# Kernel tuning notes

Hardware: AMD Instinct MI355X
Metric: run time of the kernel (lower is better)

The kernel has to match this reference:

```python
import jax, jax.numpy as jnp
import numpy as np

B, S, E, H, VS, VT = 128, 256, 512, 512, 32000, 32000


def _lstm_layer(x, mask, Wih, Whh, bih, bhh):
    # x: (S,B,E_in), mask: (S,B) bool. PyTorch gate order i,f,g,o.
    h0 = jnp.zeros((x.shape[1], Whh.shape[1]), x.dtype)
    c0 = h0
    def step(carry, inp):
        h, c = carry
        xt, mt = inp
        g = xt @ Wih.T + h @ Whh.T + bih + bhh
        i, f, gg, o = jnp.split(g, 4, axis=-1)
        i = jax.nn.sigmoid(i); f = jax.nn.sigmoid(f)
        gg = jnp.tanh(gg); o = jax.nn.sigmoid(o)
        c_new = f * c + i * gg
        h_new = o * jnp.tanh(c_new)
        m = mt[:, None]
        h2 = jnp.where(m, h_new, h)
        c2 = jnp.where(m, c_new, c)
        return (h2, c2), jnp.where(m, h_new, 0.0)  # pad_packed zero-pads
    (hT, cT), ys = jax.lax.scan(step, (h0, c0), (x, mask))
    return ys, cT


def setup_inputs() -> dict:
    key = jax.random.key(0)
    ks = jax.random.split(key, 32)
    def w(k, shape, fan_in):
        bound = 1.0 / np.sqrt(fan_in)
        return jax.random.uniform(k, shape, jnp.float32, -bound, bound)
    src_tokens = jax.random.randint(ks[0], (B, S), 0, VS)
    src_lens = jnp.sort(jax.random.randint(ks[1], (B,), S // 2, S + 1))[::-1]
    src_lens = src_lens.at[0].set(S)  # pack_padded expects descending, max = S
    trg_tokens = jax.random.randint(ks[2], (B,), 0, VT)
    inp = {
        'src_tokens': src_tokens, 'src_lens': src_lens, 'trg_tokens': trg_tokens,
        'src_emb': jax.random.normal(ks[3], (VS, E), jnp.float32),
        'trg_emb': jax.random.normal(ks[4], (VT, E), jnp.float32),
        'enc_Wih0': w(ks[5], (4 * H, E), H), 'enc_Whh0': w(ks[6], (4 * H, H), H),
        'enc_bih0': w(ks[7], (4 * H,), H), 'enc_bhh0': w(ks[8], (4 * H,), H),
        'enc_Wih1': w(ks[9], (4 * H, H), H), 'enc_Whh1': w(ks[10], (4 * H, H), H),
        'enc_bih1': w(ks[11], (4 * H,), H), 'enc_bhh1': w(ks[12], (4 * H,), H),
        'dec_Wih': w(ks[13], (4 * H, E + H), H), 'dec_Whh': w(ks[14], (4 * H, H), H),
        'dec_bih': w(ks[15], (4 * H,), H), 'dec_bhh': w(ks[16], (4 * H,), H),
        'W_init': w(ks[17], (H, 2 * H), 2 * H), 'b_init': w(ks[18], (H,), 2 * H),
        'W_hid': w(ks[19], (H, 2 * H), 2 * H), 'b_hid': w(ks[20], (H,), 2 * H),
        'W_out': w(ks[21], (VT, H), H), 'b_out': w(ks[22], (VT,), H),
    }
    return inp


def reference(src_tokens, src_lens, trg_tokens, src_emb, trg_emb,
              enc_Wih0, enc_Whh0, enc_bih0, enc_bhh0,
              enc_Wih1, enc_Whh1, enc_bih1, enc_bhh1,
              dec_Wih, dec_Whh, dec_bih, dec_bhh,
              W_init, b_init, W_hid, b_hid, W_out, b_out):
    # ---- encode ----
    x = src_emb[src_tokens]                       # (B,S,E)
    x = jnp.transpose(x, (1, 0, 2))               # (S,B,E)
    mask = jnp.arange(S)[:, None] < src_lens[None, :]  # (S,B)
    y0, c0f = _lstm_layer(x, mask, enc_Wih0, enc_Whh0, enc_bih0, enc_bhh0)
    y1, c1f = _lstm_layer(y0, mask, enc_Wih1, enc_Whh1, enc_bih1, enc_bhh1)
    src_states = jnp.transpose(y1, (1, 0, 2))     # (B,S,H)
    # final cell states (num_layers,B,H) -> (B, num_layers*H)
    final_cells = jnp.concatenate([c0f, c1f], axis=-1)  # (B,2H)
    c_dec = final_cells @ W_init.T + b_init       # (B,H)
    h_dec = jnp.tanh(c_dec)
    # ---- one decoder step ----
    emb_t = trg_emb[trg_tokens]                   # (B,E)
    vec = jnp.concatenate([emb_t, jnp.zeros((B, H), emb_t.dtype)], axis=-1)
    g = vec @ dec_Wih.T + h_dec @ dec_Whh.T + dec_bih + dec_bhh
    i, f, gg, o = jnp.split(g, 4, axis=-1)
    c = jax.nn.sigmoid(f) * c_dec + jax.nn.sigmoid(i) * jnp.tanh(gg)
    h = jax.nn.sigmoid(o) * jnp.tanh(c)           # (B,H)
    # ---- masked dot attention ----
    scores = jnp.einsum('bsh,bh->bs', src_states, h)
    smask = jnp.arange(S)[None, :] < src_lens[:, None]
    scores = jnp.where(smask, scores, -jnp.inf)
    attw = jax.nn.softmax(scores, axis=-1)
    context = jnp.einsum('bs,bsh->bh', attw, src_states)
    attn_vec = jnp.concatenate([h, context], axis=-1) @ W_hid.T + b_hid
    logits = attn_vec @ W_out.T + b_out
    prd_token = jnp.argmax(logits, axis=-1)       # softmax is monotone
    return context, h, prd_token
```

## Files before the change

kernel.cpp:

```cpp
#include <hip/hip_runtime.h>
#include <stdint.h>


typedef _Float16 f16;
typedef f16 f16x8 __attribute__((ext_vector_type(8)));
typedef float f32x4 __attribute__((ext_vector_type(4)));

#define LOSCALE 2048.0f
#define LOINV   (1.0f/2048.0f)

#define B_  128
#define S_  256
#define H_  512

__device__ __forceinline__ uint16_t hbits(f16 h){ union{ f16 f; uint16_t u; } c; c.f=h; return c.u; }

__device__ __forceinline__ uint32_t split_ph2(float x){
  f16 h = (f16)x;
  float r = (x - (float)h) * LOSCALE;
  return (uint32_t)hbits(h) | ((uint32_t)hbits((f16)r) << 16);
}
__device__ __forceinline__ float ph2val(uint32_t p){
  union{ uint16_t u; f16 f; } a, b; a.u = (uint16_t)p; b.u = (uint16_t)(p>>16);
  return (float)a.f + (float)b.f * LOINV;
}

__device__ __forceinline__ void pack_hi_lo(const uint4& a, const uint4& b, uint4& hi, uint4& lo){
  hi = make_uint4((a.x & 0xffffu) | (a.y << 16),
                  (a.z & 0xffffu) | (a.w << 16),
                  (b.x & 0xffffu) | (b.y << 16),
                  (b.z & 0xffffu) | (b.w << 16));
  lo = make_uint4((a.x >> 16) | (a.y & 0xffff0000u),
                  (a.z >> 16) | (a.w & 0xffff0000u),
                  (b.x >> 16) | (b.y & 0xffff0000u),
                  (b.z >> 16) | (b.w & 0xffff0000u));
}

__device__ __forceinline__ void split_pack8(const float* x, uint4& hi, uint4& lo){
  uint16_t h[8], l[8];
#pragma unroll
  for (int e = 0; e < 8; ++e) {
    f16 hh = (f16)x[e];
    float r = (x[e] - (float)hh) * LOSCALE;
    h[e] = hbits(hh); l[e] = hbits((f16)r);
  }
  hi = make_uint4((uint32_t)h[0]|((uint32_t)h[1]<<16), (uint32_t)h[2]|((uint32_t)h[3]<<16),
                  (uint32_t)h[4]|((uint32_t)h[5]<<16), (uint32_t)h[6]|((uint32_t)h[7]<<16));
  lo = make_uint4((uint32_t)l[0]|((uint32_t)l[1]<<16), (uint32_t)l[2]|((uint32_t)l[3]<<16),
// ... 5 lines not shown
      __builtin_bit_cast(f16x8, a), __builtin_bit_cast(f16x8, b), c, 0, 0, 0);
}

__device__ __forceinline__ float sigm(float x){ return 1.0f/(1.0f + expf(-x)); }
__device__ __forceinline__ float fsigm(float x){ return 1.0f/(1.0f + __expf(-x)); }
__device__ __forceinline__ float ftanh(float x){
  float ax = fabsf(x);
  float e = __expf(-2.0f*ax);
  float r = (1.0f - e)/(1.0f + e);
  return copysignf(r, x);
}

__device__ __forceinline__ uint32_t plane_word(uint32_t p, uint32_t pp, int odd){
  return odd ? ((pp >> 16) | (p & 0xffff0000u))
             : ((p & 0xffffu) | (pp << 16));
}

__device__ __forceinline__ size_t fl_idx(int row, int k){
  return (size_t)(k >> 5) * 4096 + (size_t)(row >> 4) * 512 + (size_t)(k & 1) * 256
       + (size_t)((k >> 3) & 3) * 64 + (size_t)(row & 15) * 4 + (size_t)((k & 7) >> 1);
}

__device__ __forceinline__ void gload_lds16(const uint32_t* gbase, uint32_t* lbase, int lane){
#if __has_builtin(__builtin_amdgcn_global_load_lds)
  __builtin_amdgcn_global_load_lds(
      (const __attribute__((address_space(1))) uint32_t*)(gbase + lane*4),
      (__attribute__((address_space(3))) uint32_t*)lbase, 16, 0, 0);
#else
  *(uint4*)(lbase + lane*4) = *(const uint4*)(gbase + lane*4);
#endif
}

__global__ __launch_bounds__(256) void k_embed_src_fl(const int* __restrict__ tok,
    const float* __restrict__ emb, uint32_t* __restrict__ out)
{
  const size_t total = (size_t)S_ * B_ * H_;
  for (size_t i = (size_t)blockIdx.x*256 + threadIdx.x; i < total; i += (size_t)gridDim.x*256) {
    int s = (int)(i >> 16), b = (int)((i >> 9) & 127), k = (int)(i & 511);
    int t = tok[b*S_ + s];
    uint32_t p = split_ph2(emb[(size_t)t*H_ + k]);
    uint32_t pp = __shfl_xor(p, 1);
    out[(size_t)s*65536 + fl_idx(b, k)] = plane_word(p, pp, k & 1);
  }
}

__global__ __launch_bounds__(256) void k_embed_trg(const int* __restrict__ tok,
    const float* __restrict__ emb, uint32_t* __restrict__ out)
{
  int i = blockIdx.x*256 + threadIdx.x;
  int e = i & (H_-1), b = i >> 9;
  int t = tok[b];
  out[i] = split_ph2(emb[(size_t)t*H_ + e]);
}

__global__ __launch_bounds__(256) void k_packW(const float* __restrict__ W,
    uint32_t* __restrict__ out)
{
  int i = blockIdx.x*256 + threadIdx.x;
  int n = i >> 9, k = i & 511;
  uint32_t p = split_ph2(W[i]);
  uint32_t pp = __shfl_xor(p, 1);
  out[(size_t)(n >> 7)*65536 + fl_idx(n & 127, k)] = plane_word(p, pp, k & 1);
}

__global__ __launch_bounds__(256) void k_packAfl(const float* __restrict__ a,
    uint32_t* __restrict__ out)
{
  int i = blockIdx.x*256 + threadIdx.x;
  int b = i >> 9, k = i & 511;
  uint32_t p = split_ph2(a[i]);
  uint32_t pp = __shfl_xor(p, 1);
  out[fl_idx(b, k)] = plane_word(p, pp, k & 1);
}

__global__ __launch_bounds__(256,2) void k_gemm_fl(
    const uint32_t* __restrict__ Afl,
    const uint32_t* __restrict__ Wfl,
    const float* __restrict__ b0, const float* __restrict__ b1,
    float* __restrict__ C, int N, int addC)
{
  __shared__ uint8_t sm[65536];
  const int tid = threadIdx.x, lane = tid & 63, wv = tid >> 6;
  const int wm = wv >> 1, wn = wv & 1;
  const int bn0 = blockIdx.x * 128, bm0 = blockIdx.y * 128;
  const uint32_t* Ab = Afl + (size_t)blockIdx.y * 65536;
  const uint32_t* Wb = Wfl + (size_t)blockIdx.x * 65536;

  f32x4 acc0[4][4], acc1[4][4];
#pragma unroll
  for (int i = 0; i < 4; ++i)
#pragma unroll
    for (int j = 0; j < 4; ++j) { acc0[i][j] = (f32x4){0,0,0,0}; acc1[i][j] = (f32x4){0,0,0,0}; }

  for (int it = 0; it < 8; ++it) {
    __syncthreads();
    {
      const uint32_t* gsrc = (wv < 2 ? Ab : Wb) + (size_t)it*8192 + (size_t)(wv & 1)*4096;
      uint32_t* lb = (uint32_t*)(sm + (size_t)wv*16384);
#pragma unroll
      for (int e = 0; e < 16; ++e)
        gload_lds16(gsrc + e*256, lb + e*256, lane);
    }
    asm volatile("s_waitcnt vmcnt(0)" ::: "memory");
    __syncthreads();

#pragma unroll
    for (int kt = 0; kt < 2; ++kt) {
      uint4 ah[4], al[4];
#pragma unroll
      for (int i = 0; i < 4; ++i) {
        const uint8_t* p = sm + (size_t)(kt*8 + wm*4 + i)*2048 + lane*16;
        ah[i] = *(const uint4*)p; al[i] = *(const uint4*)(p + 1024);
      }
#pragma unroll
      for (int j = 0; j < 4; ++j) {
        const uint8_t* p = sm + 32768 + (size_t)(kt*8 + wn*4 + j)*2048 + lane*16;
        uint4 bh = *(const uint4*)p;
        uint4 bl = *(const uint4*)(p + 1024);
#pragma unroll
        for (int i = 0; i < 4; ++i) {
          acc0[i][j] = mfma16(ah[i], bh, acc0[i][j]);
          acc1[i][j] = mfma16(al[i], bh, acc1[i][j]);
          acc1[i][j] = mfma16(ah[i], bl, acc1[i][j]);
        }
      }
    }
  }

#pragma unroll
  for (int i = 0; i < 4; ++i) {
    int row0 = bm0 + (wm*4+i)*16 + ((lane>>4)<<2);
#pragma unroll
    for (int j = 0; j < 4; ++j) {
      int col = bn0 + (wn*4+j)*16 + (lane & 15);
      float bias = 0.f;
      if (b0) bias += b0[col];
      if (b1) bias += b1[col];
      f32x4 v = acc0[i][j] + acc1[i][j] * LOINV;
#pragma unroll
      for (int r = 0; r < 4; ++r) {
        size_t idx = (size_t)(row0 + r) * N + col;
        float out = v[r] + bias;
        if (addC) out += C[idx];
        C[idx] = out;
      }
    }
  }
}

__global__ __launch_bounds__(256,2) void k_gemm(
    const uint32_t* __restrict__ A, int lda,
    const float* __restrict__ W, int ldw,
    const float* __restrict__ b0, const float* __restrict__ b1,
    float* __restrict__ C, int N, int K, int addC)
{
  __shared__ uint8_t sm[65536];
  const int tid = threadIdx.x;
  const int lane = tid & 63, wv = tid >> 6;
  const int wm = wv >> 1, wn = wv & 1;
  const int bn0 = blockIdx.x * 128, bm0 = blockIdx.y * 128;

  const int srow = tid >> 1;
  const int skh  = (tid & 1) * 32;
  const int smt  = srow >> 4, sr = srow & 15, skt = tid & 1;

  f32x4 acc0[4][4], acc1[4][4];
#pragma unroll
  for (int i = 0; i < 4; ++i)
#pragma unroll
    for (int j = 0; j < 4; ++j) { acc0[i][j] = (f32x4){0,0,0,0}; acc1[i][j] = (f32x4){0,0,0,0}; }

  for (int k0 = 0; k0 < K; k0 += 64) {
    __syncthreads();
    {
      const uint32_t* ap = A + (size_t)(bm0 + srow) * lda + (k0 + skh);
      uint4 q[8];
#pragma unroll
// ... 34 lines not shown
        uint4 bh = *(const uint4*)p;
        uint4 bl = *(const uint4*)(p + 1024);
#pragma unroll
        for (int i = 0; i < 4; ++i) {
          acc0[i][j] = mfma16(ah[i], bh, acc0[i][j]);
          acc1[i][j] = mfma16(al[i], bh, acc1[i][j]);
          acc1[i][j] = mfma16(ah[i], bl, acc1[i][j]);
        }
      }
    }
  }

#pragma unroll
  for (int i = 0; i < 4; ++i) {
    int row0 = bm0 + (wm*4+i)*16 + ((lane>>4)<<2);
#pragma unroll
    for (int j = 0; j < 4; ++j) {
      int col = bn0 + (wn*4+j)*16 + (lane & 15);
      float bias = 0.f;
      if (b0) bias += b0[col];
      if (b1) bias += b1[col];
      f32x4 v = acc0[i][j] + acc1[i][j] * LOINV;
#pragma unroll
      for (int r = 0; r < 4; ++r) {
        size_t idx = (size_t)(row0 + r) * N + col;
        float out = v[r] + bias;
        if (addC) out += C[idx];
        C[idx] = out;
      }
    }
  }
}

__global__ __launch_bounds__(256,1) void k_lstm2(
    const float* __restrict__ Whh0, const float* __restrict__ Whh1,
    const float* __restrict__ bih1, const float* __restrict__ bhh1,
    const float* __restrict__ xg,
    const int*  __restrict__ lens,
    uint32_t* __restrict__ mb0,
    uint32_t* __restrict__ mb1,
    float* __restrict__ cb0, float* __restrict__ cb1,
    uint32_t* __restrict__ y1buf,
    uint32_t* __restrict__ flg0, uint32_t* __restrict__ flg1,
    const uint32_t* __restrict__ Wp1,
    int s0, int nt)
{
  __shared__ uint8_t sm[163840];
  uint8_t* wih = sm;
  uint8_t* tile = sm + 131072;
  uint64_t* tile64 = (uint64_t*)tile;
  float* g0ex = (float*)tile;
  float* g1ex = (float*)(tile + 4096);

  const int tid = threadIdx.x, lane = tid & 63, wv = tid >> 6;
  const int bg = blockIdx.x & 7, hs = blockIdx.x >> 3;
  const int row = lane & 15, qh = lane >> 4;

  {
    const uint32_t* wpb = Wp1 + (size_t)(wv*4 + (hs >> 3))*65536 + (size_t)(hs & 7)*512;
    uint32_t* lb = (uint32_t*)(wih + (size_t)wv*32768);
#pragma unroll
    for (int kt = 0; kt < 16; ++kt) {
      gload_lds16(wpb + kt*4096,       lb + kt*512,       lane);
      gload_lds16(wpb + kt*4096 + 256, lb + kt*512 + 256, lane);
    }
  }

  uint4 w0h[16], w0l[16], w1h[16], w1l[16];
  {
    const float* r0 = Whh0 + (size_t)(wv*512 + hs*16 + row)*512 + qh*8;
    const float* r1 = Whh1 + (size_t)(wv*512 + hs*16 + row)*512 + qh*8;
#pragma unroll
    for (int kt = 0; kt < 16; ++kt) {
      float xs[8];
      float4 v0 = *(const float4*)(r0 + kt*32), v1 = *(const float4*)(r0 + kt*32 + 4);
      xs[0]=v0.x; xs[1]=v0.y; xs[2]=v0.z; xs[3]=v0.w;
      xs[4]=v1.x; xs[5]=v1.y; xs[6]=v1.z; xs[7]=v1.w;
      split_pack8(xs, w0h[kt], w0l[kt]);
      v0 = *(const float4*)(r1 + kt*32); v1 = *(const float4*)(r1 + kt*32 + 4);
      xs[0]=v0.x; xs[1]=v0.y; xs[2]=v0.z; xs[3]=v0.w;
      xs[4]=v1.x; xs[5]=v1.y; xs[6]=v1.z; xs[7]=v1.w;
      split_pack8(xs, w1h[kt], w1l[kt]);
    }
  }

  const int b_l = tid >> 4, uu = tid & 15;
  const int bglob = bg*16 + b_l;
  const size_t bgoff = (size_t)bg*8192;
  const int oct_p = hs*2 + (uu >> 3);
  const size_t widx = (size_t)b_l*512 + (size_t)(uu & 1)*256
                    + ((size_t)(oct_p ^ b_l) << 2) + (size_t)((uu & 7) >> 1);
  const int len_b = lens[bglob];
  const int lenA  = lens[bg*16 + row];
  float c0_reg = cb0[(size_t)bglob*512 + hs*16 + uu];
  float c1_reg = cb1[(size_t)bglob*512 + hs*16 + uu];
  float h0_reg, h1_reg;
  {
    size_t ib = (size_t)(s0 & 1)*65536 + bgoff + (size_t)b_l*512
              + ((size_t)(oct_p ^ b_l) << 2) + (size_t)((uu & 7) >> 1);
    uint32_t hiw = mb0[ib], low = mb0[ib + 256];
    int sh = (uu & 1) * 16;
    union{ uint16_t u; f16 f; } ch, cl;
    ch.u = (uint16_t)(hiw >> sh); cl.u = (uint16_t)(low >> sh);
    h0_reg = (float)ch.f + (float)cl.f * LOINV;
    int s1i = (s0 >= 1) ? (s0 - 1) : 0;
    size_t ib1 = (size_t)(s1i & 1)*65536 + bgoff + (size_t)b_l*512
               + ((size_t)(oct_p ^ b_l) << 2) + (size_t)((uu & 7) >> 1);
    hiw = mb1[ib1]; low = mb1[ib1 + 256];
    ch.u = (uint16_t)(hiw >> sh); cl.u = (uint16_t)(low >> sh);
    h1_reg = (float)ch.f + (float)cl.f * LOINV;
  }
  float b1g[4];
#pragma unroll
  for (int g = 0; g < 4; ++g)
    b1g[g] = bih1[g*512 + hs*16 + uu] + bhh1[g*512 + hs*16 + uu];
  const size_t yfl = (size_t)(hs >> 1)*4096 + (size_t)bg*512 + (size_t)(uu & 1)*256
                   + (size_t)((((hs & 1) << 1) | (uu >> 3)))*64 + (size_t)b_l*4
                   + (size_t)((uu & 7) >> 1);

  asm volatile("s_waitcnt vmcnt(0)" ::: "memory");
  __syncthreads();

  for (int it = 0; it < nt; ++it) {
    const int t = s0 + it;
    const bool aL0 = (t < 256);
    const bool aL1 = (t > 0);

    float xv0 = 0.f, xv1 = 0.f, xv2 = 0.f, xv3 = 0.f;
    if (aL0) {
      const float* xgp = xg + ((size_t)it*128 + bglob)*2048 + hs*16 + uu;
      xv0 = xgp[0]; xv1 = xgp[512]; xv2 = xgp[1024]; xv3 = xgp[1536];
    }

    if (it > 0) {
      if (wv == 0) {
        const uint32_t* fp = flg0 + bg*32 + (lane & 31);
        while (1) {
          uint32_t f = __hip_atomic_load(fp, __ATOMIC_RELAXED, __HIP_MEMORY_SCOPE_SYSTEM);
          if (__all((int)(f >= (uint32_t)t))) break;
          __builtin_amdgcn_s_sleep(1);
        }
      } else if (wv == 1) {
        const uint32_t* fp = flg1 + bg*32 + (lane & 31);
        while (1) {
          uint32_t f = __hip_atomic_load(fp, __ATOMIC_RELAXED, __HIP_MEMORY_SCOPE_SYSTEM);
          if (__all((int)(f >= (uint32_t)(t - 1)))) break;
          __builtin_amdgcn_s_sleep(1);
        }
      }
    }
    __builtin_amdgcn_s_barrier();
    __builtin_amdgcn_sched_barrier(0);

    const uint64_t* sp0 = (const uint64_t*)(mb0 + (size_t)(t & 1)*65536 + bgoff);
    const uint64_t* sp1 = (const uint64_t*)(mb1 + (size_t)((t - 1) & 1)*65536 + bgoff);
    uint64_t v0[16], v1[16];
#pragma unroll
    for (int e = 0; e < 16; ++e)
      v0[e] = __hip_atomic_load(sp0 + tid + e*256, __ATOMIC_RELAXED, __HIP_MEMORY_SCOPE_SYSTEM);
    if (aL1) {
#pragma unroll
      for (int e = 0; e < 16; ++e)
        v1[e] = __hip_atomic_load(sp1 + tid + e*256, __ATOMIC_RELAXED, __HIP_MEMORY_SCOPE_SYSTEM);
    }
#pragma unroll
    for (int e = 0; e < 16; ++e)
      tile64[tid + e*256] = v0[e];
    asm volatile("s_waitcnt lgkmcnt(0)" ::: "memory");
    __builtin_amdgcn_s_barrier();
    __builtin_amdgcn_sched_barrier(0);

    f32x4 A0 = (f32x4){0,0,0,0}, A1 = (f32x4){0,0,0,0}, A2 = (f32x4){0,0,0,0};
    f32x4 B0 = (f32x4){0,0,0,0}, B1 = (f32x4){0,0,0,0}, B2 = (f32x4){0,0,0,0};
    {
      const uint8_t* hrp = tile + (size_t)row*2048;
      const uint8_t* wbase = wih + (size_t)wv*32768;
      const bool cY = aL1 && ((t - 1) < lenA);
      const uint4 z4 = make_uint4(0,0,0,0);
#pragma unroll
      for (int kt = 0; kt < 16; ++kt) {
        int oct = kt*4 + qh;
        const uint8_t* pA = hrp + (((oct ^ row)) << 4);
        uint4 ah = *(const uint4*)pA, al = *(const uint4*)(pA + 1024);
        A0 = mfma16(ah, w0h[kt], A0);
        A1 = mfma16(al, w0h[kt], A1);
        A2 = mfma16(ah, w0l[kt], A2);
        uint4 yh = cY ? ah : z4, yl = cY ? al : z4;
        const uint8_t* pB = wbase + (size_t)kt*2048 + lane*16;
        uint4 bh = *(const uint4*)pB, bl = *(const uint4*)(pB + 1024);
        B0 = mfma16(yh, bh, B0);
        B1 = mfma16(yl, bh, B1);
        B2 = mfma16(yh, bl, B2);
      }
    }
    __builtin_amdgcn_sched_barrier(0);
    __builtin_amdgcn_s_barrier();
    __builtin_amdgcn_sched_barrier(0);

    if (aL1) {
#pragma unroll
      for (int e = 0; e < 16; ++e)
        tile64[tid + e*256] = v1[e];
    }
    asm volatile("s_waitcnt lgkmcnt(0)" ::: "memory");
    __builtin_amdgcn_s_barrier();
    __builtin_amdgcn_sched_barrier(0);

    if (aL1) {
      const uint8_t* hrp = tile + (size_t)row*2048;
#pragma unroll
      for (int kt = 0; kt < 16; ++kt) {
        int oct = kt*4 + qh;
        const uint8_t* pA = hrp + (((oct ^ row)) << 4);
        uint4 ah = *(const uint4*)pA, al = *(const uint4*)(pA + 1024);
        B0 = mfma16(ah, w1h[kt], B0);
        B1 = mfma16(al, w1h[kt], B1);
        B2 = mfma16(ah, w1l[kt], B2);
      }
    }
    __builtin_amdgcn_sched_barrier(0);
    __builtin_amdgcn_s_barrier();
    __builtin_amdgcn_sched_barrier(0);

    {
      int col = lane & 15, rb = (lane >> 4) << 2;
      if (aL0) {
#pragma unroll
        for (int r = 0; r < 4; ++r)
          g0ex[(size_t)(wv*16 + rb + r)*16 + col] = A0[r] + (A1[r] + A2[r])*LOINV;
      }
      if (aL1) {
#pragma unroll
        for (int r = 0; r < 4; ++r)
          g1ex[(size_t)(wv*16 + rb + r)*16 + col] = B0[r] + (B1[r] + B2[r])*LOINV;
      }
    }
    asm volatile("s_waitcnt lgkmcnt(0)" ::: "memory");
    __builtin_amdgcn_s_barrier();
    __builtin_amdgcn_sched_barrier(0);

    uint32_t p1w = 0; bool m1 = false;
    if (aL0) {
      float gi = g0ex[(size_t)(0*16 + b_l)*16 + uu] + xv0;
      float gf = g0ex[(size_t)(1*16 + b_l)*16 + uu] + xv1;
      float gg = g0ex[(size_t)(2*16 + b_l)*16 + uu] + xv2;
      float go = g0ex[(size_t)(3*16 + b_l)*16 + uu] + xv3;
      float cn = fsigm(gf)*c0_reg + fsigm(gi)*ftanh(gg);
      float hn = fsigm(go)*ftanh(cn);
      bool m = (t < len_b);
      c0_reg = m ? cn : c0_reg;
      h0_reg = m ? hn : h0_reg;
      uint32_t p = split_ph2(h0_reg);
      uint32_t pp = __shfl_xor(p, 1);
      __hip_atomic_store(mb0 + (size_t)((t + 1) & 1)*65536 + bgoff + widx,
                         plane_word(p, pp, uu & 1), __ATOMIC_RELAXED, __HIP_MEMORY_SCOPE_SYSTEM);
    }
    if (aL1) {
      float gi = g1ex[(size_t)(0*16 + b_l)*16 + uu] + b1g[0];
      float gf = g1ex[(size_t)(1*16 + b_l)*16 + uu] + b1g[1];
      float gg = g1ex[(size_t)(2*16 + b_l)*16 + uu] + b1g[2];
      float go = g1ex[(size_t)(3*16 + b_l)*16 + uu] + b1g[3];
      float cn = fsigm(gf)*c1_reg + fsigm(gi)*ftanh(gg);
      float hn = fsigm(go)*ftanh(cn);
      m1 = ((t - 1) < len_b);
      c1_reg = m1 ? cn : c1_reg;
      h1_reg = m1 ? hn : h1_reg;
      uint32_t p = split_ph2(h1_reg);
      uint32_t pp = __shfl_xor(p, 1);
      p1w = plane_word(p, pp, uu & 1);
      __hip_atomic_store(mb1 + (size_t)(t & 1)*65536 + bgoff + widx,
                         p1w, __ATOMIC_RELAXED, __HIP_MEMORY_SCOPE_SYSTEM);
    }
    asm volatile("s_waitcnt vmcnt(0)" ::: "memory");
    __builtin_amdgcn_s_barrier();
    __builtin_amdgcn_sched_barrier(0);
    if (tid == 0) {
      if (aL0) __hip_atomic_store(flg0 + bg*32 + hs, (uint32_t)(t + 1),
                                  __ATOMIC_RELAXED, __HIP_MEMORY_SCOPE_SYSTEM);
      if (aL1) __hip_atomic_store(flg1 + bg*32 + hs, (uint32_t)t,
                                  __ATOMIC_RELAXED, __HIP_MEMORY_SCOPE_SYSTEM);
    }
    if (aL1) y1buf[(size_t)(t - 1)*65536 + yfl] = m1 ? p1w : 0u;
  }
  cb0[(size_t)bglob*512 + hs*16 + uu] = c0_reg;
  cb1[(size_t)bglob*512 + hs*16 + uu] = c1_reg;
}

__global__ __launch_bounds__(256) void k_pack2(const float* __restrict__ a,
    const float* __restrict__ b, uint32_t* __restrict__ out)
{
  int i = blockIdx.x*256 + threadIdx.x;
  int bb = i >> 10, k = i & 1023;
  float x = (k < 512) ? a[(size_t)bb*512 + k] : b[(size_t)bb*512 + k - 512];
  out[i] = split_ph2(x);
}

__global__ __launch_bounds__(256) void k_tanh_split(const float* __restrict__ c,
    uint32_t* __restrict__ hp)
{ int i = blockIdx.x*256 + threadIdx.x; hp[i] = split_ph2(tanhf(c[i])); }

__global__ __launch_bounds__(256) void k_dec_cell(const float* __restrict__ g,
    const float* __restrict__ cdec, float* __restrict__ hout, float* __restrict__ dh)
{
  int i = blockIdx.x*256 + threadIdx.x;
  int b = i >> 9, u = i & 511;
  const float* gb = g + (size_t)b*2048;
  float c = sigm(gb[512 + u])*cdec[i] + sigm(gb[u])*tanhf(gb[1024 + u]);
  float h = sigm(gb[1536 + u])*tanhf(c);
  hout[i] = h; dh[i] = h;
}

__global__ __launch_bounds__(256) void k_attn(const uint32_t* __restrict__ y1,
    const float* __restrict__ h, const int* __restrict__ lens,
    float* __restrict__ ctx, float* __restrict__ dctx)
{
  __shared__ float hsh[512];
  __shared__ float sc[256];
  __shared__ float red[8];
  const int b = blockIdx.x, tid = threadIdx.x, lane = tid & 63, wv = tid >> 6;
  hsh[tid]       = h[(size_t)b*512 + tid];
  hsh[tid + 256] = h[(size_t)b*512 + tid + 256];
  const int len = lens[b];
  __syncthreads();

  const size_t lanebase = (size_t)(lane >> 2)*4096 + (size_t)(b >> 4)*512
                        + (size_t)(lane & 3)*64 + (size_t)(b & 15)*4;
  for (int it = 0; it < 64; ++it) {
    int s = wv*64 + it;
    const uint32_t* yb = y1 + (size_t)s*65536 + lanebase;
    uint4 hw = *(const uint4*)yb;
    uint4 lw = *(const uint4*)(yb + 256);
    int k0 = lane*8;
    uint32_t hws[4] = {hw.x,hw.y,hw.z,hw.w}, lws[4] = {lw.x,lw.y,lw.z,lw.w};
    float d = 0.f;
#pragma unroll
    for (int w = 0; w < 4; ++w) {
      union{uint16_t u; f16 f;} h0,h1,l0,l1;
      h0.u=(uint16_t)hws[w]; h1.u=(uint16_t)(hws[w]>>16);
      l0.u=(uint16_t)lws[w]; l1.u=(uint16_t)(lws[w]>>16);
      d += ((float)h0.f + (float)l0.f*LOINV) * hsh[k0 + 2*w]
         + ((float)h1.f + (float)l1.f*LOINV) * hsh[k0 + 2*w + 1];
    }
    for (int off = 32; off; off >>= 1) d += __shfl_xor(d, off);
    if (lane == 0) sc[s] = d;
  }
  __syncthreads();

  float v = (tid < len) ? sc[tid] : -INFINITY;
  float mx = v;
  for (int off = 32; off; off >>= 1) mx = fmaxf(mx, __shfl_xor(mx, off));
  if (lane == 0) red[wv] = mx;
  __syncthreads();
  mx = fmaxf(fmaxf(red[0], red[1]), fmaxf(red[2], red[3]));
  float e = (tid < len) ? expf(v - mx) : 0.f;
  float ssum = e;
  for (int off = 32; off; off >>= 1) ssum += __shfl_xor(ssum, off);
  if (lane == 0) red[4 + wv] = ssum;
  __syncthreads();
  float tot = red[4] + red[5] + red[6] + red[7];
  __syncthreads();
  sc[tid] = e / tot;
  __syncthreads();

  const int u0 = tid, u1 = tid + 256;
  const size_t bu0 = (size_t)(u0 >> 5)*4096 + (size_t)(b >> 4)*512
                   + (size_t)((u0 >> 3) & 3)*64 + (size_t)(b & 15)*4 + (size_t)((u0 & 7) >> 1);
  const size_t bu1 = (size_t)(u1 >> 5)*4096 + (size_t)(b >> 4)*512
                   + (size_t)((u1 >> 3) & 3)*64 + (size_t)(b & 15)*4 + (size_t)((u1 & 7) >> 1);
  const int sh = (tid & 1) * 16;
  float acc0 = 0.f, acc1 = 0.f;
  for (int s = 0; s < 256; ++s) {
    float w = sc[s];
    const uint32_t* yb = y1 + (size_t)s*65536;
    uint32_t hi0 = yb[bu0], lo0 = yb[bu0 + 256];
    uint32_t hi1 = yb[bu1], lo1 = yb[bu1 + 256];
    union{uint16_t u; f16 f;} a,b2,c2,d2;
    a.u =(uint16_t)(hi0 >> sh); b2.u=(uint16_t)(lo0 >> sh);
    c2.u=(uint16_t)(hi1 >> sh); d2.u=(uint16_t)(lo1 >> sh);
    acc0 += w*((float)a.f  + (float)b2.f*LOINV);
    acc1 += w*((float)c2.f + (float)d2.f*LOINV);
  }
  ctx [(size_t)b*512 + tid]       = acc0;  ctx [(size_t)b*512 + tid + 256] = acc1;
  dctx[(size_t)b*512 + tid]       = acc0;  dctx[(size_t)b*512 + tid + 256] = acc1;
}

__global__ __launch_bounds__(256) void k_argmax(const float* __restrict__ logits,
    float* __restrict__ out)
{
  __shared__ float bv[256];
  __shared__ int   bi[256];
  const int b = blockIdx.x, tid = threadIdx.x;
  const float* L = logits + (size_t)b*32000;
  float best = -INFINITY; int idx = 0;
  for (int i = tid; i < 32000; i += 256) {
    float v = L[i];
    if (v > best) { best = v; idx = i; }
  }
  bv[tid] = best; bi[tid] = idx;
  __syncthreads();
  for (int sft = 128; sft; sft >>= 1) {
    if (tid < sft) {
      if (bv[tid+sft] > bv[tid] || (bv[tid+sft] == bv[tid] && bi[tid+sft] < bi[tid])) {
        bv[tid] = bv[tid+sft]; bi[tid] = bi[tid+sft];
      }
    }
    __syncthreads();
  }
  if (tid == 0) out[b] = (float)bi[0];
}

extern "C" void kernel_launch(void* const* d_in, const int* in_sizes, int n_in,
                              void* d_out, int out_size, void* d_ws, size_t ws_size,
                              hipStream_t stream)
{
  (void)in_sizes; (void)n_in; (void)out_size; (void)ws_size;
  const int*   src_tokens = (const int*)  d_in[0];
  const int*   src_lens   = (const int*)  d_in[1];
  const int*   trg_tokens = (const int*)  d_in[2];
  const float* src_emb    = (const float*)d_in[3];
  const float* trg_emb    = (const float*)d_in[4];
  const float* Wih0 = (const float*)d_in[5];
  const float* Whh0 = (const float*)d_in[6];
  const float* bih0 = (const float*)d_in[7];
  const float* bhh0 = (const float*)d_in[8];
  const float* Wih1 = (const float*)d_in[9];
  const float* Whh1 = (const float*)d_in[10];
  const float* bih1 = (const float*)d_in[11];
  const float* bhh1 = (const float*)d_in[12];
  const float* dWih = (const float*)d_in[13];
  const float* dWhh = (const float*)d_in[14];
  const float* dbih = (const float*)d_in[15];
  const float* dbhh = (const float*)d_in[16];
  const float* Winit= (const float*)d_in[17];
  const float* binit= (const float*)d_in[18];
  const float* Whid = (const float*)d_in[19];
  const float* bhid = (const float*)d_in[20];
  const float* Wout = (const float*)d_in[21];
  const float* bout = (const float*)d_in[22];

  uint8_t* ws = (uint8_t*)d_ws;
  constexpr size_t MBs = 1ull << 20;
  constexpr size_t OFF_AP    = 0;
  constexpr size_t OFF_Y1    = 64*MBs;
  constexpr size_t OFF_XG    = 128*MBs;
  constexpr size_t OFF_MB    = 192*MBs;
  constexpr size_t OFF_CB0   = OFF_MB    + 1*MBs;
  constexpr size_t OFF_CB1   = OFF_CB0   + 256*1024;
  constexpr size_t OFF_FLG   = OFF_CB1   + 256*1024;
  constexpr size_t OFF_PK    = OFF_FLG   + 4096;
  constexpr size_t OFF_CDEC  = OFF_PK    + 512*1024;
  constexpr size_t OFF_HDECP = OFF_CDEC  + 256*1024;
  constexpr size_t OFF_EMBP  = OFF_HDECP + 256*1024;
  constexpr size_t OFF_G     = OFF_EMBP  + 256*1024;
  constexpr size_t OFF_HDEC2 = OFF_G     + 1*MBs;
  constexpr size_t OFF_CTX   = OFF_HDEC2 + 256*1024;
  constexpr size_t OFF_AVEC  = OFF_CTX   + 256*1024;
  constexpr size_t OFF_AVECP = OFF_AVEC  + 256*1024;
  constexpr size_t OFF_LOG   = OFF_AVECP + 256*1024;

  uint32_t* Ap    = (uint32_t*)(ws + OFF_AP);
  uint32_t* Y1    = (uint32_t*)(ws + OFF_Y1);
  float*    Xg    = (float*)   (ws + OFF_XG);
  uint32_t* WoutF = (uint32_t*)(ws + OFF_XG);
  uint32_t* mb0   = (uint32_t*)(ws + OFF_MB);
  uint32_t* mb1   = (uint32_t*)(ws + OFF_MB + 512*1024);
  float*    cb0   = (float*)   (ws + OFF_CB0);
  float*    cb1   = (float*)   (ws + OFF_CB1);
  uint32_t* flg0  = (uint32_t*)(ws + OFF_FLG);
  uint32_t* flg1  = (uint32_t*)(ws + OFF_FLG + 2048);
  uint32_t* pk    = (uint32_t*)(ws + OFF_PK);
  float*    cdec  = (float*)   (ws + OFF_CDEC);
  uint32_t* hdecp = (uint32_t*)(ws + OFF_HDECP);
  uint32_t* embp  = (uint32_t*)(ws + OFF_EMBP);
  float*    g     = (float*)   (ws + OFF_G);
  float*    hdec2 = (float*)   (ws + OFF_HDEC2);
  float*    ctx   = (float*)   (ws + OFF_CTX);
  float*    avec  = (float*)   (ws + OFF_AVEC);
  uint32_t* avecp = (uint32_t*)(ws + OFF_AVECP);
  float*    logit = (float*)   (ws + OFF_LOG);
  uint32_t* Wp0   = (uint32_t*)(ws + OFF_LOG);
  uint32_t* Wp1   = (uint32_t*)(ws + OFF_LOG + 4*MBs);
  float*    dout  = (float*)   d_out;

  k_packW<<<4096, 256, 0, stream>>>(Wih0, Wp0);
  k_packW<<<4096, 256, 0, stream>>>(Wih1, Wp1);

  hipMemsetAsync(mb0,  0, 1024*1024, stream);
  hipMemsetAsync(flg0, 0, 4096, stream);
  hipMemsetAsync(cb0,  0, 65536*4, stream);
  hipMemsetAsync(cb1,  0, 65536*4, stream);
  k_embed_src_fl<<<2048, 256, 0, stream>>>(src_tokens, src_emb, Ap);
  for (int c = 0; c < 4; ++c) {
    int s0 = c * 64;
    k_gemm_fl<<<dim3(16, 64), 256, 0, stream>>>(Ap + (size_t)s0*65536,
        Wp0, bih0, bhh0, Xg, 2048, 0);
    k_lstm2<<<256, 256, 0, stream>>>(Whh0, Whh1, bih1, bhh1, Xg, src_lens,
        mb0, mb1, cb0, cb1, Y1, flg0, flg1, Wp1, s0, (c == 3) ? 65 : 64);
  }

  k_packW<<<64000, 256, 0, stream>>>(Wout, WoutF);

  k_pack2<<<512, 256, 0, stream>>>(cb0, cb1, pk);
  k_gemm<<<dim3(4, 1), 256, 0, stream>>>(pk, 1024, Winit, 1024, binit, nullptr,
      cdec, 512, 1024, 0);
  k_tanh_split<<<256, 256, 0, stream>>>(cdec, hdecp);

  k_embed_trg<<<256, 256, 0, stream>>>(trg_tokens, trg_emb, embp);
  k_gemm<<<dim3(16, 1), 256, 0, stream>>>(embp, 512, dWih, 1024, dbih, dbhh,
      g, 2048, 512, 0);
  k_gemm<<<dim3(16, 1), 256, 0, stream>>>(hdecp, 512, dWhh, 512, nullptr, nullptr,
      g, 2048, 512, 1);
  k_dec_cell<<<256, 256, 0, stream>>>(g, cdec, hdec2, dout + 65536);

  k_attn<<<128, 256, 0, stream>>>(Y1, hdec2, src_lens, ctx, dout);

  k_pack2<<<512, 256, 0, stream>>>(hdec2, ctx, pk);
  k_gemm<<<dim3(4, 1), 256, 0, stream>>>(pk, 1024, Whid, 1024, bhid, nullptr,
      avec, 512, 1024, 0);
  k_packAfl<<<256, 256, 0, stream>>>(avec, avecp);
  k_gemm_fl<<<dim3(250, 1), 256, 0, stream>>>(avecp, WoutF, bout, nullptr,
      logit, 32000, 0);
  k_argmax<<<128, 256, 0, stream>>>(logit, dout + 131072);
}
```

Measured before the change: 2.484 ms.

## Hoist layer-1 input projection into batched GEMM with skewed chunk pipeline

```diff
diff --git a/kernel.cpp b/kernel.cpp
--- a/kernel.cpp
+++ b/kernel.cpp
@@ -14,6 +14,7 @@
 #define H_  512
 
 __device__ __forceinline__ uint16_t hbits(f16 h){ union{ f16 f; uint16_t u; } c; c.f=h; return c.u; }
+__device__ __forceinline__ float f16val(uint16_t u){ union{ uint16_t u; f16 f; } c; c.u=u; return (float)c.f; }
 
 __device__ __forceinline__ uint32_t split_ph2(float x){
   f16 h = (f16)x;
@@ -85,15 +86,15 @@
 }
 
 __global__ __launch_bounds__(256) void k_embed_src_fl(const int* __restrict__ tok,
-    const float* __restrict__ emb, uint32_t* __restrict__ out)
-{
-  const size_t total = (size_t)S_ * B_ * H_;
+    const float* __restrict__ emb, uint32_t* __restrict__ out, int s0)
+{
+  const size_t total = (size_t)64 * B_ * H_;
   for (size_t i = (size_t)blockIdx.x*256 + threadIdx.x; i < total; i += (size_t)gridDim.x*256) {
-    int s = (int)(i >> 16), b = (int)((i >> 9) & 127), k = (int)(i & 511);
-    int t = tok[b*S_ + s];
+    int sblk = (int)(i >> 16), b = (int)((i >> 9) & 127), k = (int)(i & 511);
+    int t = tok[b*S_ + (s0 + sblk)];
     uint32_t p = split_ph2(emb[(size_t)t*H_ + k]);
     uint32_t pp = __shfl_xor(p, 1);
-    out[(size_t)s*65536 + fl_idx(b, k)] = plane_word(p, pp, k & 1);
+    out[(size_t)sblk*65536 + fl_idx(b, k)] = plane_word(p, pp, k & 1);
   }
 }
 
@@ -130,7 +131,7 @@
     const uint32_t* __restrict__ Afl,
     const uint32_t* __restrict__ Wfl,
     const float* __restrict__ b0, const float* __restrict__ b1,
-    float* __restrict__ C, int N, int addC)
+    float* __restrict__ C, int N, int addC, int outMode)
 {
   __shared__ uint8_t sm[65536];
   const int tid = threadIdx.x, lane = tid & 63, wv = tid >> 6;
@@ -195,7 +196,8 @@
         size_t idx = (size_t)(row0 + r) * N + col;
         float out = v[r] + bias;
         if (addC) out += C[idx];
-        C[idx] = out;
+        if (outMode == 2) ((uint16_t*)C)[idx] = hbits((f16)out);
+        else              C[idx] = out;
       }
     }
   }
@@ -296,21 +298,21 @@
   }
 }
 
-__global__ __launch_bounds__(256,1) void k_lstm2(
-    const float* __restrict__ Whh0, const float* __restrict__ Whh1,
-    const float* __restrict__ bih1, const float* __restrict__ bhh1,
-    const float* __restrict__ xg,
-    const int*  __restrict__ lens,
-    uint32_t* __restrict__ mb0,
-    uint32_t* __restrict__ mb1,
+__global__ __launch_bounds__(256,1) void k_lstm2v2(
+    const float* __restrict__ Whh0,
+    const uint32_t* __restrict__ Wph1,
+    const uint16_t* __restrict__ xg0,
+    const uint16_t* __restrict__ xg1,
+    const int* __restrict__ lens,
+    uint32_t* __restrict__ mb0, uint32_t* __restrict__ mb1,
     float* __restrict__ cb0, float* __restrict__ cb1,
+    uint32_t* __restrict__ y0buf,
     uint32_t* __restrict__ y1buf,
     uint32_t* __restrict__ flg0, uint32_t* __restrict__ flg1,
-    const uint32_t* __restrict__ Wp1,
-    int s0, int nt)
+    int s0L0, int s0L1, int doL0, int doL1)
 {
   __shared__ uint8_t sm[163840];
-  uint8_t* wih = sm;
+  uint8_t* whh1 = sm;
   uint8_t* tile = sm + 131072;
   uint64_t* tile64 = (uint64_t*)tile;
   float* g0ex = (float*)tile;
@@ -321,8 +323,8 @@
   const int row = lane & 15, qh = lane >> 4;
 
   {
-    const uint32_t* wpb = Wp1 + (size_t)(wv*4 + (hs >> 3))*65536 + (size_t)(hs & 7)*512;
-    uint32_t* lb = (uint32_t*)(wih + (size_t)wv*32768);
+    const uint32_t* wpb = Wph1 + (size_t)(wv*4 + (hs >> 3))*65536 + (size_t)(hs & 7)*512;
+    uint32_t* lb = (uint32_t*)(whh1 + (size_t)wv*32768);
 #pragma unroll
     for (int kt = 0; kt < 16; ++kt) {
       gload_lds16(wpb + kt*4096,       lb + kt*512,       lane);
@@ -330,10 +332,9 @@
     }
   }
 
-  uint4 w0h[16], w0l[16], w1h[16], w1l[16];
+  uint4 w0h[16], w0l[16];
   {
     const float* r0 = Whh0 + (size_t)(wv*512 + hs*16 + row)*512 + qh*8;
-    const float* r1 = Whh1 + (size_t)(wv*512 + hs*16 + row)*512 + qh*8;
 #pragma unroll
     for (int kt = 0; kt < 16; ++kt) {
       float xs[8];
@@ -341,10 +342,6 @@
       xs[0]=v0.x; xs[1]=v0.y; xs[2]=v0.z; xs[3]=v0.w;
       xs[4]=v1.x; xs[5]=v1.y; xs[6]=v1.z; xs[7]=v1.w;
       split_pack8(xs, w0h[kt], w0l[kt]);
-      v0 = *(const float4*)(r1 + kt*32); v1 = *(const float4*)(r1 + kt*32 + 4);
-      xs[0]=v0.x; xs[1]=v0.y; xs[2]=v0.z; xs[3]=v0.w;
-      xs[4]=v1.x; xs[5]=v1.y; xs[6]=v1.z; xs[7]=v1.w;
-      split_pack8(xs, w1h[kt], w1l[kt]);
     }
   }
 
@@ -355,29 +352,19 @@
   const size_t widx = (size_t)b_l*512 + (size_t)(uu & 1)*256
                     + ((size_t)(oct_p ^ b_l) << 2) + (size_t)((uu & 7) >> 1);
   const int len_b = lens[bglob];
-  const int lenA  = lens[bg*16 + row];
   float c0_reg = cb0[(size_t)bglob*512 + hs*16 + uu];
   float c1_reg = cb1[(size_t)bglob*512 + hs*16 + uu];
   float h0_reg, h1_reg;
   {
-    size_t ib = (size_t)(s0 & 1)*65536 + bgoff + (size_t)b_l*512
-              + ((size_t)(oct_p ^ b_l) << 2) + (size_t)((uu & 7) >> 1);
-    uint32_t hiw = mb0[ib], low = mb0[ib + 256];
-    int sh = (uu & 1) * 16;
-    union{ uint16_t u; f16 f; } ch, cl;
-    ch.u = (uint16_t)(hiw >> sh); cl.u = (uint16_t)(low >> sh);
-    h0_reg = (float)ch.f + (float)cl.f * LOINV;
-    int s1i = (s0 >= 1) ? (s0 - 1) : 0;
-    size_t ib1 = (size_t)(s1i & 1)*65536 + bgoff + (size_t)b_l*512
-               + ((size_t)(oct_p ^ b_l) << 2) + (size_t)((uu & 7) >> 1);
+    const size_t ibs = (size_t)b_l*512 + ((size_t)(oct_p ^ b_l) << 2) + (size_t)((uu & 7) >> 1);
+    const int sh = (uu & 1) * 16;
+    size_t ib0 = (size_t)(s0L0 & 1)*65536 + bgoff + ibs;
+    uint32_t hiw = mb0[ib0], low = mb0[ib0 + 256];
+    h0_reg = f16val((uint16_t)(hiw >> sh)) + f16val((uint16_t)(low >> sh)) * LOINV;
+    size_t ib1 = (size_t)(s0L1 & 1)*65536 + bgoff + ibs;
     hiw = mb1[ib1]; low = mb1[ib1 + 256];
-    ch.u = (uint16_t)(hiw >> sh); cl.u = (uint16_t)(low >> sh);
-    h1_reg = (float)ch.f + (float)cl.f * LOINV;
-  }
-  float b1g[4];
-#pragma unroll
-  for (int g = 0; g < 4; ++g)
-    b1g[g] = bih1[g*512 + hs*16 + uu] + bhh1[g*512 + hs*16 + uu];
+    h1_reg = f16val((uint16_t)(hiw >> sh)) + f16val((uint16_t)(low >> sh)) * LOINV;
+  }
   const size_t yfl = (size_t)(hs >> 1)*4096 + (size_t)bg*512 + (size_t)(uu & 1)*256
                    + (size_t)((((hs & 1) << 1) | (uu >> 3)))*64 + (size_t)b_l*4
                    + (size_t)((uu & 7) >> 1);
@@ -385,62 +372,63 @@
   asm volatile("s_waitcnt vmcnt(0)" ::: "memory");
   __syncthreads();
 
-  for (int it = 0; it < nt; ++it) {
-    const int t = s0 + it;
-    const bool aL0 = (t < 256);
-    const bool aL1 = (t > 0);
-
-    float xv0 = 0.f, xv1 = 0.f, xv2 = 0.f, xv3 = 0.f;
-    if (aL0) {
-      const float* xgp = xg + ((size_t)it*128 + bglob)*2048 + hs*16 + uu;
-      xv0 = xgp[0]; xv1 = xgp[512]; xv2 = xgp[1024]; xv3 = xgp[1536];
-    }
-
-    if (it > 0) {
-      if (wv == 0) {
-        const uint32_t* fp = flg0 + bg*32 + (lane & 31);
-        while (1) {
-          uint32_t f = __hip_atomic_load(fp, __ATOMIC_RELAXED, __HIP_MEMORY_SCOPE_SYSTEM);
-          if (__all((int)(f >= (uint32_t)t))) break;
-          __builtin_amdgcn_s_sleep(1);
-        }
-      } else if (wv == 1) {
-        const uint32_t* fp = flg1 + bg*32 + (lane & 31);
-        while (1) {
-          uint32_t f = __hip_atomic_load(fp, __ATOMIC_RELAXED, __HIP_MEMORY_SCOPE_SYSTEM);
-          if (__all((int)(f >= (uint32_t)(t - 1)))) break;
-          __builtin_amdgcn_s_sleep(1);
-        }
+  for (int it = 0; it < 64; ++it) {
+    const int tL0 = s0L0 + it, tL1 = s0L1 + it;
+
+    uint16_t x0w[4] = {0,0,0,0}, x1w[4] = {0,0,0,0};
+    if (doL0) {
+      const uint16_t* xp = xg0 + ((size_t)it*128 + bglob)*2048 + hs*16 + uu;
+      x0w[0]=xp[0]; x0w[1]=xp[512]; x0w[2]=xp[1024]; x0w[3]=xp[1536];
+    }
+    if (doL1) {
+      const uint16_t* xp = xg1 + ((size_t)it*128 + bglob)*2048 + hs*16 + uu;
+      x1w[0]=xp[0]; x1w[1]=xp[512]; x1w[2]=xp[1024]; x1w[3]=xp[1536];
+    }
+
+    if (doL0 && tL0 > 0 && wv == 0) {
+      const uint32_t* fp = flg0 + bg*32 + (lane & 31);
+      while (1) {
+        uint32_t f = __hip_atomic_load(fp, __ATOMIC_RELAXED, __HIP_MEMORY_SCOPE_SYSTEM);
+        if (__all((int)(f >= (uint32_t)tL0))) break;
+        __builtin_amdgcn_s_sleep(1);
+      }
+    }
+    if (doL1 && tL1 > 0 && wv == 1) {
+      const uint32_t* fp = flg1 + bg*32 + (lane & 31);
+      while (1) {
+        uint32_t f = __hip_atomic_load(fp, __ATOMIC_RELAXED, __HIP_MEMORY_SCOPE_SYSTEM);
+        if (__all((int)(f >= (uint32_t)tL1))) break;
+        __builtin_amdgcn_s_sleep(1);
       }
     }
     __builtin_amdgcn_s_barrier();
     __builtin_amdgcn_sched_barrier(0);
 
-    const uint64_t* sp0 = (const uint64_t*)(mb0 + (size_t)(t & 1)*65536 + bgoff);
-    const uint64_t* sp1 = (const uint64_t*)(mb1 + (size_t)((t - 1) & 1)*65536 + bgoff);
-    uint64_t v0[16], v1[16];
-#pragma unroll
-    for (int e = 0; e < 16; ++e)
-      v0[e] = __hip_atomic_load(sp0 + tid + e*256, __ATOMIC_RELAXED, __HIP_MEMORY_SCOPE_SYSTEM);
-    if (aL1) {
+    uint64_t v0[16];
+    if (doL0) {
+      const uint64_t* sp0 = (const uint64_t*)(mb0 + (size_t)(tL0 & 1)*65536 + bgoff);
+#pragma unroll
+      for (int e = 0; e < 16; ++e)
+        v0[e] = __hip_atomic_load(sp0 + tid + e*256, __ATOMIC_RELAXED, __HIP_MEMORY_SCOPE_SYSTEM);
+#pragma unroll
+      for (int e = 0; e < 16; ++e)
+        tile64[tid + e*256] = v0[e];
+    }
+    uint64_t v1[16];
+    if (doL1) {
+      const uint64_t* sp1 = (const uint64_t*)(mb1 + (size_t)(tL1 & 1)*65536 + bgoff);
 #pragma unroll
       for (int e = 0; e < 16; ++e)
         v1[e] = __hip_atomic_load(sp1 + tid + e*256, __ATOMIC_RELAXED, __HIP_MEMORY_SCOPE_SYSTEM);
     }
-#pragma unroll
-    for (int e = 0; e < 16; ++e)
-      tile64[tid + e*256] = v0[e];
     asm volatile("s_waitcnt lgkmcnt(0)" ::: "memory");
     __builtin_amdgcn_s_barrier();
     __builtin_amdgcn_sched_barrier(0);
 
     f32x4 A0 = (f32x4){0,0,0,0}, A1 = (f32x4){0,0,0,0}, A2 = (f32x4){0,0,0,0};
     f32x4 B0 = (f32x4){0,0,0,0}, B1 = (f32x4){0,0,0,0}, B2 = (f32x4){0,0,0,0};
-    {
+    if (doL0) {
       const uint8_t* hrp = tile + (size_t)row*2048;
-      const uint8_t* wbase = wih + (size_t)wv*32768;
-      const bool cY = aL1 && ((t - 1) < lenA);
-      const uint4 z4 = make_uint4(0,0,0,0);
 #pragma unroll
       for (int kt = 0; kt < 16; ++kt) {
         int oct = kt*4 + qh;
@@ -449,19 +437,13 @@
         A0 = mfma16(ah, w0h[kt], A0);
         A1 = mfma16(al, w0h[kt], A1);
         A2 = mfma16(ah, w0l[kt], A2);
-        uint4 yh = cY ? ah : z4, yl = cY ? al : z4;
-        const uint8_t* pB = wbase + (size_t)kt*2048 + lane*16;
-        uint4 bh = *(const uint4*)pB, bl = *(const uint4*)(pB + 1024);
-        B0 = mfma16(yh, bh, B0);
-        B1 = mfma16(yl, bh, B1);
-        B2 = mfma16(yh, bl, B2);
       }
     }
     __builtin_amdgcn_sched_barrier(0);
     __builtin_amdgcn_s_barrier();
     __builtin_amdgcn_sched_barrier(0);
 
-    if (aL1) {
+    if (doL1) {
 #pragma unroll
       for (int e = 0; e < 16; ++e)
         tile64[tid + e*256] = v1[e];
@@ -470,16 +452,19 @@
     __builtin_amdgcn_s_barrier();
     __builtin_amdgcn_sched_barrier(0);
 
-    if (aL1) {
+    if (doL1) {
       const uint8_t* hrp = tile + (size_t)row*2048;
+      const uint8_t* wbase = whh1 + (size_t)wv*32768;
 #pragma unroll
       for (int kt = 0; kt < 16; ++kt) {
         int oct = kt*4 + qh;
         const uint8_t* pA = hrp + (((oct ^ row)) << 4);
         uint4 ah = *(const uint4*)pA, al = *(const uint4*)(pA + 1024);
-        B0 = mfma16(ah, w1h[kt], B0);
-        B1 = mfma16(al, w1h[kt], B1);
-        B2 = mfma16(ah, w1l[kt], B2);
+        const uint8_t* pB = wbase + (size_t)kt*2048 + lane*16;
+        uint4 bh = *(const uint4*)pB, bl = *(const uint4*)(pB + 1024);
+        B0 = mfma16(ah, bh, B0);
+        B1 = mfma16(al, bh, B1);
+        B2 = mfma16(ah, bl, B2);
       }
     }
     __builtin_amdgcn_sched_barrier(0);
@@ -488,12 +473,12 @@
 
     {
       int col = lane & 15, rb = (lane >> 4) << 2;
-      if (aL0) {
+      if (doL0) {
 #pragma unroll
         for (int r = 0; r < 4; ++r)
           g0ex[(size_t)(wv*16 + rb + r)*16 + col] = A0[r] + (A1[r] + A2[r])*LOINV;
       }
-      if (aL1) {
+      if (doL1) {
 #pragma unroll
         for (int r = 0; r < 4; ++r)
           g1ex[(size_t)(wv*16 + rb + r)*16 + col] = B0[r] + (B1[r] + B2[r])*LOINV;
@@ -503,48 +488,50 @@
     __builtin_amdgcn_s_barrier();
     __builtin_amdgcn_sched_barrier(0);
 
-    uint32_t p1w = 0; bool m1 = false;
-    if (aL0) {
-      float gi = g0ex[(size_t)(0*16 + b_l)*16 + uu] + xv0;
-      float gf = g0ex[(size_t)(1*16 + b_l)*16 + uu] + xv1;
-      float gg = g0ex[(size_t)(2*16 + b_l)*16 + uu] + xv2;
-      float go = g0ex[(size_t)(3*16 + b_l)*16 + uu] + xv3;
+    uint32_t p0w = 0, p1w = 0; bool m0 = false, m1 = false;
+    if (doL0) {
+      float gi = g0ex[(size_t)(0*16 + b_l)*16 + uu] + f16val(x0w[0]);
+      float gf = g0ex[(size_t)(1*16 + b_l)*16 + uu] + f16val(x0w[1]);
+      float gg = g0ex[(size_t)(2*16 + b_l)*16 + uu] + f16val(x0w[2]);
+      float go = g0ex[(size_t)(3*16 + b_l)*16 + uu] + f16val(x0w[3]);
       float cn = fsigm(gf)*c0_reg + fsigm(gi)*ftanh(gg);
       float hn = fsigm(go)*ftanh(cn);
-      bool m = (t < len_b);
-      c0_reg = m ? cn : c0_reg;
-      h0_reg = m ? hn : h0_reg;
+      m0 = (tL0 < len_b);
+      c0_reg = m0 ? cn : c0_reg;
+      h0_reg = m0 ? hn : h0_reg;
       uint32_t p = split_ph2(h0_reg);
       uint32_t pp = __shfl_xor(p, 1);
-      __hip_atomic_store(mb0 + (size_t)((t + 1) & 1)*65536 + bgoff + widx,
-                         plane_word(p, pp, uu & 1), __ATOMIC_RELAXED, __HIP_MEMORY_SCOPE_SYSTEM);
-    }
-    if (aL1) {
-      float gi = g1ex[(size_t)(0*16 + b_l)*16 + uu] + b1g[0];
-      float gf = g1ex[(size_t)(1*16 + b_l)*16 + uu] + b1g[1];
-      float gg = g1ex[(size_t)(2*16 + b_l)*16 + uu] + b1g[2];
-      float go = g1ex[(size_t)(3*16 + b_l)*16 + uu] + b1g[3];
+      p0w = plane_word(p, pp, uu & 1);
+      __hip_atomic_store(mb0 + (size_t)((tL0 + 1) & 1)*65536 + bgoff + widx,
+                         p0w, __ATOMIC_RELAXED, __HIP_MEMORY_SCOPE_SYSTEM);
+    }
+    if (doL1) {
+      float gi = g1ex[(size_t)(0*16 + b_l)*16 + uu] + f16val(x1w[0]);
+      float gf = g1ex[(size_t)(1*16 + b_l)*16 + uu] + f16val(x1w[1]);
+      float gg = g1ex[(size_t)(2*16 + b_l)*16 + uu] + f16val(x1w[2]);
+      float go = g1ex[(size_t)(3*16 + b_l)*16 + uu] + f16val(x1w[3]);
       float cn = fsigm(gf)*c1_reg + fsigm(gi)*ftanh(gg);
       float hn = fsigm(go)*ftanh(cn);
-      m1 = ((t - 1) < len_b);
+      m1 = (tL1 < len_b);
       c1_reg = m1 ? cn : c1_reg;
       h1_reg = m1 ? hn : h1_reg;
       uint32_t p = split_ph2(h1_reg);
       uint32_t pp = __shfl_xor(p, 1);
       p1w = plane_word(p, pp, uu & 1);
-      __hip_atomic_store(mb1 + (size_t)(t & 1)*65536 + bgoff + widx,
+      __hip_atomic_store(mb1 + (size_t)((tL1 + 1) & 1)*65536 + bgoff + widx,
                          p1w, __ATOMIC_RELAXED, __HIP_MEMORY_SCOPE_SYSTEM);
     }
     asm volatile("s_waitcnt vmcnt(0)" ::: "memory");
     __builtin_amdgcn_s_barrier();
     __builtin_amdgcn_sched_barrier(0);
     if (tid == 0) {
-      if (aL0) __hip_atomic_store(flg0 + bg*32 + hs, (uint32_t)(t + 1),
-                                  __ATOMIC_RELAXED, __HIP_MEMORY_SCOPE_SYSTEM);
-      if (aL1) __hip_atomic_store(flg1 + bg*32 + hs, (uint32_t)t,
-                                  __ATOMIC_RELAXED, __HIP_MEMORY_SCOPE_SYSTEM);
-    }
-    if (aL1) y1buf[(size_t)(t - 1)*65536 + yfl] = m1 ? p1w : 0u;
+      if (doL0) __hip_atomic_store(flg0 + bg*32 + hs, (uint32_t)(tL0 + 1),
+                                   __ATOMIC_RELAXED, __HIP_MEMORY_SCOPE_SYSTEM);
+      if (doL1) __hip_atomic_store(flg1 + bg*32 + hs, (uint32_t)(tL1 + 1),
+                                   __ATOMIC_RELAXED, __HIP_MEMORY_SCOPE_SYSTEM);
+    }
+    if (doL0) y0buf[(size_t)it*65536 + yfl] = m0 ? p0w : 0u;
+    if (doL1) y1buf[(size_t)tL1*65536 + yfl] = m1 ? p1w : 0u;
   }
   cb0[(size_t)bglob*512 + hs*16 + uu] = c0_reg;
   cb1[(size_t)bglob*512 + hs*16 + uu] = c1_reg;
@@ -599,11 +586,8 @@
     float d = 0.f;
 #pragma unroll
     for (int w = 0; w < 4; ++w) {
-      union{uint16_t u; f16 f;} h0,h1,l0,l1;
-      h0.u=(uint16_t)hws[w]; h1.u=(uint16_t)(hws[w]>>16);
-      l0.u=(uint16_t)lws[w]; l1.u=(uint16_t)(lws[w]>>16);
-      d += ((float)h0.f + (float)l0.f*LOINV) * hsh[k0 + 2*w]
-         + ((float)h1.f + (float)l1.f*LOINV) * hsh[k0 + 2*w + 1];
+      d += (f16val((uint16_t)hws[w]) + f16val((uint16_t)lws[w])*LOINV) * hsh[k0 + 2*w]
+         + (f16val((uint16_t)(hws[w]>>16)) + f16val((uint16_t)(lws[w]>>16))*LOINV) * hsh[k0 + 2*w + 1];
     }
     for (int off = 32; off; off >>= 1) d += __shfl_xor(d, off);
     if (lane == 0) sc[s] = d;
@@ -638,11 +622,8 @@
     const uint32_t* yb = y1 + (size_t)s*65536;
     uint32_t hi0 = yb[bu0], lo0 = yb[bu0 + 256];
     uint32_t hi1 = yb[bu1], lo1 = yb[bu1 + 256];
-    union{uint16_t u; f16 f;} a,b2,c2,d2;
-    a.u =(uint16_t)(hi0 >> sh); b2.u=(uint16_t)(lo0 >> sh);
-    c2.u=(uint16_t)(hi1 >> sh); d2.u=(uint16_t)(lo1 >> sh);
-    acc0 += w*((float)a.f  + (float)b2.f*LOINV);
-    acc1 += w*((float)c2.f + (float)d2.f*LOINV);
+    acc0 += w*(f16val((uint16_t)(hi0 >> sh)) + f16val((uint16_t)(lo0 >> sh))*LOINV);
+    acc1 += w*(f16val((uint16_t)(hi1 >> sh)) + f16val((uint16_t)(lo1 >> sh))*LOINV);
   }
   ctx [(size_t)b*512 + tid]       = acc0;  ctx [(size_t)b*512 + tid + 256] = acc1;
   dctx[(size_t)b*512 + tid]       = acc0;  dctx[(size_t)b*512 + tid + 256] = acc1;
@@ -704,11 +685,13 @@
 
   uint8_t* ws = (uint8_t*)d_ws;
   constexpr size_t MBs = 1ull << 20;
-  constexpr size_t OFF_AP    = 0;
-  constexpr size_t OFF_Y1    = 64*MBs;
-  constexpr size_t OFF_XG    = 128*MBs;
-  constexpr size_t OFF_MB    = 192*MBs;
-  constexpr size_t OFF_CB0   = OFF_MB    + 1*MBs;
+  constexpr size_t OFF_APR   = 0;
+  constexpr size_t OFF_XG0   = 16*MBs;
+  constexpr size_t OFF_XG1   = 48*MBs;
+  constexpr size_t OFF_Y0    = 80*MBs;
+  constexpr size_t OFF_Y1    = 96*MBs;
+  constexpr size_t OFF_MB    = 160*MBs;
+  constexpr size_t OFF_CB0   = 161*MBs;
   constexpr size_t OFF_CB1   = OFF_CB0   + 256*1024;
   constexpr size_t OFF_FLG   = OFF_CB1   + 256*1024;
   constexpr size_t OFF_PK    = OFF_FLG   + 4096;
@@ -720,12 +703,17 @@
   constexpr size_t OFF_CTX   = OFF_HDEC2 + 256*1024;
   constexpr size_t OFF_AVEC  = OFF_CTX   + 256*1024;
   constexpr size_t OFF_AVECP = OFF_AVEC  + 256*1024;
-  constexpr size_t OFF_LOG   = OFF_AVECP + 256*1024;
-
-  uint32_t* Ap    = (uint32_t*)(ws + OFF_AP);
+  constexpr size_t OFF_WP0   = 166*MBs;
+  constexpr size_t OFF_WP1   = 170*MBs;
+  constexpr size_t OFF_WPH1  = 174*MBs;
+
+  uint32_t* Apr   = (uint32_t*)(ws + OFF_APR);
+  uint16_t* Xg0h  = (uint16_t*)(ws + OFF_XG0);
+  uint16_t* Xg1h  = (uint16_t*)(ws + OFF_XG1);
+  uint32_t* Y0    = (uint32_t*)(ws + OFF_Y0);
   uint32_t* Y1    = (uint32_t*)(ws + OFF_Y1);
-  float*    Xg    = (float*)   (ws + OFF_XG);
-  uint32_t* WoutF = (uint32_t*)(ws + OFF_XG);
+  uint32_t* WoutF = (uint32_t*)(ws + OFF_APR);
+  float*    logit = (float*)   (ws + OFF_Y1);
   uint32_t* mb0   = (uint32_t*)(ws + OFF_MB);
   uint32_t* mb1   = (uint32_t*)(ws + OFF_MB + 512*1024);
   float*    cb0   = (float*)   (ws + OFF_CB0);
@@ -741,25 +729,31 @@
   float*    ctx   = (float*)   (ws + OFF_CTX);
   float*    avec  = (float*)   (ws + OFF_AVEC);
   uint32_t* avecp = (uint32_t*)(ws + OFF_AVECP);
-  float*    logit = (float*)   (ws + OFF_LOG);
-  uint32_t* Wp0   = (uint32_t*)(ws + OFF_LOG);
-  uint32_t* Wp1   = (uint32_t*)(ws + OFF_LOG + 4*MBs);
+  uint32_t* Wp0   = (uint32_t*)(ws + OFF_WP0);
+  uint32_t* Wp1   = (uint32_t*)(ws + OFF_WP1);
+  uint32_t* Wph1  = (uint32_t*)(ws + OFF_WPH1);
   float*    dout  = (float*)   d_out;
 
   k_packW<<<4096, 256, 0, stream>>>(Wih0, Wp0);
   k_packW<<<4096, 256, 0, stream>>>(Wih1, Wp1);
+  k_packW<<<4096, 256, 0, stream>>>(Whh1, Wph1);
 
   hipMemsetAsync(mb0,  0, 1024*1024, stream);
   hipMemsetAsync(flg0, 0, 4096, stream);
   hipMemsetAsync(cb0,  0, 65536*4, stream);
   hipMemsetAsync(cb1,  0, 65536*4, stream);
-  k_embed_src_fl<<<2048, 256, 0, stream>>>(src_tokens, src_emb, Ap);
-  for (int c = 0; c < 4; ++c) {
-    int s0 = c * 64;
-    k_gemm_fl<<<dim3(16, 64), 256, 0, stream>>>(Ap + (size_t)s0*65536,
-        Wp0, bih0, bhh0, Xg, 2048, 0);
-    k_lstm2<<<256, 256, 0, stream>>>(Whh0, Whh1, bih1, bhh1, Xg, src_lens,
-        mb0, mb1, cb0, cb1, Y1, flg0, flg1, Wp1, s0, (c == 3) ? 65 : 64);
+  for (int rc = 0; rc < 5; ++rc) {
+    if (rc < 4) {
+      k_embed_src_fl<<<2048, 256, 0, stream>>>(src_tokens, src_emb, Apr, rc*64);
+      k_gemm_fl<<<dim3(16, 64), 256, 0, stream>>>(Apr, Wp0, bih0, bhh0,
+          (float*)Xg0h, 2048, 0, 2);
+    }
+    if (rc >= 1)
+      k_gemm_fl<<<dim3(16, 64), 256, 0, stream>>>(Y0, Wp1, bih1, bhh1,
+          (float*)Xg1h, 2048, 0, 2);
+    k_lstm2v2<<<256, 256, 0, stream>>>(Whh0, Wph1, Xg0h, Xg1h, src_lens,
+        mb0, mb1, cb0, cb1, Y0, Y1, flg0, flg1,
+        rc*64, (rc - 1)*64, rc < 4 ? 1 : 0, rc >= 1 ? 1 : 0);
   }
 
   k_packW<<<64000, 256, 0, stream>>>(Wout, WoutF);
@@ -783,6 +777,6 @@
       avec, 512, 1024, 0);
   k_packAfl<<<256, 256, 0, stream>>>(avec, avecp);
   k_gemm_fl<<<dim3(250, 1), 256, 0, stream>>>(avecp, WoutF, bout, nullptr,
-      logit, 32000, 0);
+      logit, 32000, 0, 0);
   k_argmax<<<128, 256, 0, stream>>>(logit, dout + 131072);
 }
```

Result: slower. 2.613 ms (+5.2%).
